# Performance work log

Measured on AMD Instinct MI355X. Metric: run time of the kernel, lower is better.

The kernel has to match this reference:

```python
import jax, jax.numpy as jnp
import numpy as np

NEG_INF = -9e15


def setup_inputs() -> dict:
    key = jax.random.key(0)
    k1, k2, k3, k4, k5 = jax.random.split(key, 5)
    N, F_IN, F_OUT = 8192, 512, 256
    x = jax.random.normal(k1, (N, F_IN), dtype=jnp.float32)
    adjacent_matrix = jax.random.randint(k2, (N, N), 0, 2, dtype=jnp.int32)
    # xavier-normal-like scales (gain sqrt(2))
    W = jax.random.normal(k3, (F_IN, F_OUT), dtype=jnp.float32) * np.sqrt(2.0) * np.sqrt(2.0 / (F_IN + F_OUT))
    a1 = jax.random.normal(k4, (F_OUT, 1), dtype=jnp.float32) * np.sqrt(2.0) * np.sqrt(2.0 / (F_OUT + 1))
    a2 = jax.random.normal(k5, (F_OUT, 1), dtype=jnp.float32) * np.sqrt(2.0) * np.sqrt(2.0 / (F_OUT + 1))
    return {"x": x, "adjacent_matrix": adjacent_matrix, "W": W, "a1": a1, "a2": a2}


def reference(x, adjacent_matrix, W, a1, a2):
    alpha = 0.2  # LeakyReLU negative slope
    h = x @ W                                   # [N, F_out]
    f1 = h @ a1                                 # [N, 1]
    f2 = h @ a2                                 # [N, 1]
    e = f1 + f2.T                               # [N, N] broadcast pairwise scores
    e = jnp.where(e > 0, e, alpha * e)          # LeakyReLU
    e = jnp.where(adjacent_matrix > 0, e, NEG_INF)  # mask non-edges
    attention = jax.nn.softmax(e, axis=1)       # [N, N]
    h_prime = attention @ h                     # [N, F_out]
    return jax.nn.elu(h_prime)                  # concat=True -> ELU
```

## Files before the change

kernel.cpp:

```cpp
#include <hip/hip_runtime.h>
#include <hip/hip_bf16.h>

#define N_NODES 8192
#define F_IN 512
#define F_OUT 256
#define KSPLIT 4
#define KCHUNK (N_NODES / KSPLIT)

using short8 = __attribute__((ext_vector_type(8))) short;
using f32x4  = __attribute__((ext_vector_type(4))) float;

__device__ __forceinline__ short f2bf(float v) {
    union { float f; unsigned u; } x; x.f = v;
    unsigned r = x.u + 0x7fffu + ((x.u >> 16) & 1u);
    return (short)(r >> 16);
}

__global__ void k_prep(const float* __restrict__ W, const float* __restrict__ a1,
                       const float* __restrict__ a2, float* __restrict__ w1,
                       float* __restrict__ w2, short* __restrict__ WTg) {
    const int k = blockIdx.x;
    const int l = threadIdx.x;
    float4 wv = *(const float4*)(W + (size_t)k * F_OUT + 4 * l);
    float4 av = *(const float4*)(a1 + 4 * l);
    float4 bv = *(const float4*)(a2 + 4 * l);
    float s1 = wv.x*av.x + wv.y*av.y + wv.z*av.z + wv.w*av.w;
    float s2 = wv.x*bv.x + wv.y*bv.y + wv.z*bv.z + wv.w*bv.w;
    WTg[(size_t)(4*l+0)*F_IN + k] = f2bf(wv.x);
    WTg[(size_t)(4*l+1)*F_IN + k] = f2bf(wv.y);
    WTg[(size_t)(4*l+2)*F_IN + k] = f2bf(wv.z);
    WTg[(size_t)(4*l+3)*F_IN + k] = f2bf(wv.w);
    #pragma unroll
    for (int off = 32; off; off >>= 1) {
        s1 += __shfl_down(s1, off);
        s2 += __shfl_down(s2, off);
    }
    if (l == 0) { w1[k] = s1; w2[k] = s2; }
}

__global__ void k_f12(const float* __restrict__ x, const float* __restrict__ w1,
                      const float* __restrict__ w2, float* __restrict__ f1,
                      float* __restrict__ f2) {
    const int wv = threadIdx.x >> 6, l = threadIdx.x & 63;
    const int i = blockIdx.x * 4 + wv;
    const float* xr = x + (size_t)i * F_IN;
    float s1 = 0.f, s2 = 0.f;
    #pragma unroll
    for (int t = 0; t < 2; ++t) {
        int k = t * 256 + l * 4;
        float4 xv = *(const float4*)(xr + k);
        float4 u  = *(const float4*)(w1 + k);
        float4 v  = *(const float4*)(w2 + k);
        s1 += xv.x*u.x + xv.y*u.y + xv.z*u.z + xv.w*u.w;
        s2 += xv.x*v.x + xv.y*v.y + xv.z*v.z + xv.w*v.w;
    }
    #pragma unroll
    for (int off = 32; off; off >>= 1) {
        s1 += __shfl_down(s1, off);
        s2 += __shfl_down(s2, off);
    }
    if (l == 0) { f1[i] = s1; f2[i] = s2; }
}

__global__ void k_f2max(const float* __restrict__ f2, float* __restrict__ F2max) {
    const int t = threadIdx.x;
    float m = -3.4e38f;
    for (int i = t; i < N_NODES; i += 1024) m = fmaxf(m, f2[i]);
    #pragma unroll
    for (int off = 32; off; off >>= 1) m = fmaxf(m, __shfl_down(m, off));
    __shared__ float sm[16];
    if ((t & 63) == 0) sm[t >> 6] = m;
    __syncthreads();
    if (t == 0) {
        float mm = sm[0];
        #pragma unroll
        for (int w = 1; w < 16; ++w) mm = fmaxf(mm, sm[w]);
        *F2max = mm;
    }
}

__launch_bounds__(256)
__global__ void k_hT(const float* __restrict__ x, const short* __restrict__ WTg,
                     short* __restrict__ hT) {
    __shared__ short x_lds[32 * 64];
    __shared__ short wt_lds[256 * 64];
    const int tid = threadIdx.x;
    const int wv = tid >> 6, l = tid & 63, lg = l >> 4, lr = l & 15;
    const int ibase = blockIdx.x * 32;
    f32x4 acc[4][2];
    #pragma unroll
    for (int a = 0; a < 4; ++a)
        #pragma unroll
        for (int b = 0; b < 2; ++b) acc[a][b] = (f32x4){0.f, 0.f, 0.f, 0.f};
    for (int k0 = 0; k0 < F_IN; k0 += 64) {
        __syncthreads();
        {
            int i = tid >> 3, ch = tid & 7;
            const float* src = x + (size_t)(ibase + i) * F_IN + k0 + ch * 8;
            float4 v0 = *(const float4*)(src);
            float4 v1 = *(const float4*)(src + 4);
            short8 s;
            s[0]=f2bf(v0.x); s[1]=f2bf(v0.y); s[2]=f2bf(v0.z); s[3]=f2bf(v0.w);
            s[4]=f2bf(v1.x); s[5]=f2bf(v1.y); s[6]=f2bf(v1.z); s[7]=f2bf(v1.w);
            *(short8*)&x_lds[i * 64 + 8 * (ch ^ (i & 7))] = s;
        }
        {
            int cb = tid >> 3, ch = tid & 7;
            #pragma unroll
            for (int p = 0; p < 8; ++p) {
                int c = cb + 32 * p;
                short8 s = *(const short8*)(WTg + (size_t)c * F_IN + k0 + ch * 8);
                *(short8*)&wt_lds[c * 64 + 8 * (ch ^ (c & 7))] = s;
            }
        }
        __syncthreads();
        #pragma unroll
        for (int ks = 0; ks < 2; ++ks) {
            short8 bfrag[2], afrag[4];
            #pragma unroll
            for (int it = 0; it < 2; ++it) {
                int i = it * 16 + lr;
                bfrag[it] = *(short8*)&x_lds[i * 64 + 8 * ((lg + 4*ks) ^ (i & 7))];
            }
            #pragma unroll
            for (int ct = 0; ct < 4; ++ct) {
                int c = wv * 64 + ct * 16 + lr;
                afrag[ct] = *(short8*)&wt_lds[c * 64 + 8 * ((lg + 4*ks) ^ (c & 7))];
            }
            #pragma unroll
            for (int ct = 0; ct < 4; ++ct)
                #pragma unroll
                for (int it = 0; it < 2; ++it)
                    acc[ct][it] = __builtin_amdgcn_mfma_f32_16x16x32_bf16(
                        afrag[ct], bfrag[it], acc[ct][it], 0, 0, 0);
        }
    }
    #pragma unroll
    for (int ct = 0; ct < 4; ++ct)
        #pragma unroll
        for (int it = 0; it < 2; ++it)
            #pragma unroll
            for (int r = 0; r < 4; ++r) {
                int c = wv * 64 + ct * 16 + 4 * lg + r;
                int i = ibase + it * 16 + lr;
                hT[(size_t)c * N_NODES + i] = f2bf(acc[ct][it][r]);
            }
}

__launch_bounds__(256)
__global__ void k_attn(const int* __restrict__ adj, const short* __restrict__ hT,
                       const float* __restrict__ f1, const float* __restrict__ f2,
                       const float* __restrict__ F2maxp, float* __restrict__ part,
                       float* __restrict__ psum) {
    __shared__ short h_lds[256 * 64];
    const int tid = threadIdx.x;
    const int wv = tid >> 6, l = tid & 63, lg = l >> 4, lr = l & 15;
    const int ksid = blockIdx.x >> 7;
    const int rowblk = blockIdx.x & 127;
    const int r0 = rowblk * 64;
    const int myrow = r0 + wv * 16 + lr;
    const float F2m = *F2maxp;
    const float f1v = f1[myrow];
    const float e0 = f1v + F2m;
    const float cr = fmaxf(e0, 0.2f * e0);
    const float L2E = 1.44269504f;
    const float crl = cr * L2E;
    f32x4 acc[16];
    #pragma unroll
    for (int t = 0; t < 16; ++t) acc[t] = (f32x4){0.f, 0.f, 0.f, 0.f};
    float ps = 0.f;
    const int kbeg = ksid * KCHUNK;
    const int* arow = adj + (size_t)myrow * N_NODES;
    for (int k0 = kbeg; k0 < kbeg + KCHUNK; k0 += 64) {
        __syncthreads();
        {
            int cb = tid >> 3, ch = tid & 7;
            #pragma unroll
            for (int p = 0; p < 8; ++p) {
                int c = cb + 32 * p;
                short8 s = *(const short8*)(hT + (size_t)c * N_NODES + k0 + ch * 8);
                *(short8*)&h_lds[c * 64 + 8 * (ch ^ (c & 7))] = s;
            }
        }
        __syncthreads();
        #pragma unroll
        for (int ks = 0; ks < 2; ++ks) {
            const int kg = k0 + 32 * ks + 8 * lg;
            const int4 av0 = *(const int4*)(arow + kg);
            const int4 av1 = *(const int4*)(arow + kg + 4);
            const float4 fa = *(const float4*)(f2 + kg);
            const float4 fb = *(const float4*)(f2 + kg + 4);
            const float f2v[8] = {fa.x, fa.y, fa.z, fa.w, fb.x, fb.y, fb.z, fb.w};
            const int   am[8]  = {av0.x, av0.y, av0.z, av0.w, av1.x, av1.y, av1.z, av1.w};
            short8 pa;
            #pragma unroll
            for (int j = 0; j < 8; ++j) {
                float ee = f1v + f2v[j];
                float le = fmaxf(ee, 0.2f * ee);
                float pv = (am[j] > 0) ? exp2f(fmaf(le, L2E, -crl)) : 0.f;
                ps += pv;
                pa[j] = f2bf(pv);
            }
            #pragma unroll
            for (int t = 0; t < 16; ++t) {
                int c = t * 16 + lr;
                short8 bfrag = *(short8*)&h_lds[c * 64 + 8 * ((lg + 4*ks) ^ (c & 7))];
                acc[t] = __builtin_amdgcn_mfma_f32_16x16x32_bf16(pa, bfrag, acc[t], 0, 0, 0);
            }
        }
    }
    ps += __shfl_xor(ps, 16);
    ps += __shfl_xor(ps, 32);
    if (lg == 0) psum[ksid * N_NODES + myrow] = ps;
    float* pb = part + (size_t)ksid * N_NODES * F_OUT;
    #pragma unroll
    for (int t = 0; t < 16; ++t)
        #pragma unroll
        for (int r = 0; r < 4; ++r) {
            int row = r0 + wv * 16 + 4 * lg + r;
            int c = t * 16 + lr;
            pb[(size_t)row * F_OUT + c] = acc[t][r];
        }
}

__global__ void k_comb(const float* __restrict__ part, const float* __restrict__ psum,
                       float* __restrict__ out) {
    const int i = blockIdx.x, c = threadIdx.x;
    float o = 0.f, s = 0.f;
    #pragma unroll
    for (int q = 0; q < KSPLIT; ++q) {
        o += part[(size_t)q * N_NODES * F_OUT + (size_t)i * F_OUT + c];
        s += psum[q * N_NODES + i];
    }
    float v = o / s;
    out[(size_t)i * F_OUT + c] = (v > 0.f) ? v : expm1f(v);
}

extern "C" void kernel_launch(void* const* d_in, const int* in_sizes, int n_in,
                              void* d_out, int out_size, void* d_ws, size_t ws_size,
                              hipStream_t stream) {
    const float* x  = (const float*)d_in[0];
    const int* adj  = (const int*)d_in[1];
    const float* W  = (const float*)d_in[2];
    const float* a1 = (const float*)d_in[3];
    const float* a2 = (const float*)d_in[4];
    float* out = (float*)d_out;

    short* hT  = (short*)d_ws;
    short* WTg = hT + (size_t)F_OUT * N_NODES;
    float* fb  = (float*)(WTg + (size_t)F_OUT * F_IN);
    float* w1   = fb;
    float* w2   = fb + 512;
    float* f1   = fb + 1024;
    float* f2   = fb + 1024 + N_NODES;
    float* F2m  = fb + 1024 + 2 * N_NODES;
    float* part = fb + 32768;
    float* psum = part + (size_t)KSPLIT * N_NODES * F_OUT;

    k_prep<<<F_IN, 64, 0, stream>>>(W, a1, a2, w1, w2, WTg);
    k_f12<<<N_NODES / 4, 256, 0, stream>>>(x, w1, w2, f1, f2);
    k_f2max<<<1, 1024, 0, stream>>>(f2, F2m);
    k_hT<<<N_NODES / 32, 256, 0, stream>>>(x, WTg, hT);
    k_attn<<<128 * KSPLIT, 256, 0, stream>>>(adj, hT, f1, f2, F2m, part, psum);
    k_comb<<<N_NODES, 256, 0, stream>>>(part, psum, out);
}
```

Before: 454.4 us.

## Double-buffer attention tiles in registers, pack adjacency mask, drop max shift

The attention kernel now prefetches the next hT tile and adjacency chunk into registers while the current tile is computed. The adjacency values are compressed into bitmasks in LDS and loaded coalesced, replacing per-lane strided int loads. The per-row max-shift kernel is removed and exponents are clamped to 80 instead, and occupancy is hinted with launch_bounds(256,2). This adds register pressure and relies on the clamp to keep unshifted exp values from overflowing.

```diff
diff --git a/kernel.cpp b/kernel.cpp
--- a/kernel.cpp
+++ b/kernel.cpp
@@ -62,23 +62,6 @@
     if (l == 0) { f1[i] = s1; f2[i] = s2; }
 }
 
-__global__ void k_f2max(const float* __restrict__ f2, float* __restrict__ F2max) {
-    const int t = threadIdx.x;
-    float m = -3.4e38f;
-    for (int i = t; i < N_NODES; i += 1024) m = fmaxf(m, f2[i]);
-    #pragma unroll
-    for (int off = 32; off; off >>= 1) m = fmaxf(m, __shfl_down(m, off));
-    __shared__ float sm[16];
-    if ((t & 63) == 0) sm[t >> 6] = m;
-    __syncthreads();
-    if (t == 0) {
-        float mm = sm[0];
-        #pragma unroll
-        for (int w = 1; w < 16; ++w) mm = fmaxf(mm, sm[w]);
-        *F2max = mm;
-    }
-}
-
 __launch_bounds__(256)
 __global__ void k_hT(const float* __restrict__ x, const short* __restrict__ WTg,
                      short* __restrict__ hT) {
@@ -147,68 +130,109 @@
             }
 }
 
-__launch_bounds__(256)
+__launch_bounds__(256, 2)
 __global__ void k_attn(const int* __restrict__ adj, const short* __restrict__ hT,
                        const float* __restrict__ f1, const float* __restrict__ f2,
-                       const float* __restrict__ F2maxp, float* __restrict__ part,
-                       float* __restrict__ psum) {
+                       float* __restrict__ part, float* __restrict__ psum) {
     __shared__ short h_lds[256 * 64];
+    __shared__ unsigned short am_lds[64 * 4];
     const int tid = threadIdx.x;
     const int wv = tid >> 6, l = tid & 63, lg = l >> 4, lr = l & 15;
     const int ksid = blockIdx.x >> 7;
     const int rowblk = blockIdx.x & 127;
     const int r0 = rowblk * 64;
     const int myrow = r0 + wv * 16 + lr;
-    const float F2m = *F2maxp;
+    const int cb = tid >> 3, ch = tid & 7;
+    const short* hsrc = hT + (size_t)cb * N_NODES + ch * 8;
+    const int hswz = 8 * (ch ^ (cb & 7));
+    const int q = l & 3, srow = wv * 16 + (l >> 2);
+    const int* asrc = adj + (size_t)(r0 + srow) * N_NODES + q * 16;
+    const int srow4 = srow * 4 + q;
+    const int rowm4 = (wv * 16 + lr) * 4;
     const float f1v = f1[myrow];
-    const float e0 = f1v + F2m;
-    const float cr = fmaxf(e0, 0.2f * e0);
     const float L2E = 1.44269504f;
-    const float crl = cr * L2E;
     f32x4 acc[16];
     #pragma unroll
     for (int t = 0; t < 16; ++t) acc[t] = (f32x4){0.f, 0.f, 0.f, 0.f};
     float ps = 0.f;
     const int kbeg = ksid * KCHUNK;
-    const int* arow = adj + (size_t)myrow * N_NODES;
-    for (int k0 = kbeg; k0 < kbeg + KCHUNK; k0 += 64) {
+    const int kend = kbeg + KCHUNK;
+
+    short8 AH[8], BH[8];
+    int4   AA[4], BA[4];
+
+#define LOADT(K0, H, A) do {                                                   \
+    _Pragma("unroll")                                                          \
+    for (int p = 0; p < 8; ++p)                                                \
+        H[p] = *(const short8*)(hsrc + (size_t)(32 * p) * N_NODES + (K0));     \
+    _Pragma("unroll")                                                          \
+    for (int p = 0; p < 4; ++p)                                                \
+        A[p] = *(const int4*)(asrc + (K0) + p * 4);                            \
+} while (0)
+
+#define WRITET(H, A) do {                                                      \
+    _Pragma("unroll")                                                          \
+    for (int p = 0; p < 8; ++p)                                                \
+        *(short8*)&h_lds[(cb + 32 * p) * 64 + hswz] = H[p];                    \
+    unsigned m = 0;                                                            \
+    _Pragma("unroll")                                                          \
+    for (int p = 0; p < 4; ++p) {                                              \
+        m |= (A[p].x > 0 ? 1u : 0u) << (4 * p);                                \
+        m |= (A[p].y > 0 ? 2u : 0u) << (4 * p);                                \
+        m |= (A[p].z > 0 ? 4u : 0u) << (4 * p);                                \
+        m |= (A[p].w > 0 ? 8u : 0u) << (4 * p);                                \
+    }                                                                          \
+    am_lds[srow4] = (unsigned short)m;                                         \
+} while (0)
+
+#define COMPUTE(K0) do {                                                       \
+    _Pragma("unroll")                                                          \
+    for (int ks = 0; ks < 2; ++ks) {                                           \
+        const int kg = (K0) + 32 * ks + 8 * lg;                                \
+        const unsigned am = am_lds[rowm4 + 2 * ks + (lg >> 1)];                \
+        const unsigned mbyte = (am >> (8 * (lg & 1))) & 0xffu;                 \
+        const float4 fa = *(const float4*)(f2 + kg);                           \
+        const float4 fb = *(const float4*)(f2 + kg + 4);                       \
+        const float f2v[8] = {fa.x, fa.y, fa.z, fa.w, fb.x, fb.y, fb.z, fb.w}; \
+        short8 pa;                                                             \
+        _Pragma("unroll")                                                      \
+        for (int j = 0; j < 8; ++j) {                                          \
+            float ee = f1v + f2v[j];                                           \
+            float le = fmaxf(ee, 0.2f * ee);                                   \
+            float pv = (mbyte & (1u << j))                                     \
+                           ? exp2f(fminf(le * L2E, 80.f)) : 0.f;               \
+            ps += pv;                                                          \
+            pa[j] = f2bf(pv);                                                  \
+        }                                                                      \
+        _Pragma("unroll")                                                      \
+        for (int t = 0; t < 16; ++t) {                                         \
+            const int c = t * 16 + lr;                                         \
+            short8 bfrag = *(short8*)&h_lds[c * 64 + 8 * ((lg + 4*ks) ^ (lr & 7))]; \
+            acc[t] = __builtin_amdgcn_mfma_f32_16x16x32_bf16(pa, bfrag, acc[t], 0, 0, 0); \
+        }                                                                      \
+    }                                                                          \
+} while (0)
+
+    LOADT(kbeg, AH, AA);
+    for (int k0 = kbeg; k0 < kend; k0 += 128) {
+        __syncthreads();
+        WRITET(AH, AA);
+        __syncthreads();
+        LOADT(k0 + 64, BH, BA);
+        COMPUTE(k0);
+        __syncthreads();
+        WRITET(BH, BA);
         __syncthreads();
         {
-            int cb = tid >> 3, ch = tid & 7;
-            #pragma unroll
-            for (int p = 0; p < 8; ++p) {
-                int c = cb + 32 * p;
-                short8 s = *(const short8*)(hT + (size_t)c * N_NODES + k0 + ch * 8);
-                *(short8*)&h_lds[c * 64 + 8 * (ch ^ (c & 7))] = s;
-            }
-        }
-        __syncthreads();
-        #pragma unroll
-        for (int ks = 0; ks < 2; ++ks) {
-            const int kg = k0 + 32 * ks + 8 * lg;
-            const int4 av0 = *(const int4*)(arow + kg);
-            const int4 av1 = *(const int4*)(arow + kg + 4);
-            const float4 fa = *(const float4*)(f2 + kg);
-            const float4 fb = *(const float4*)(f2 + kg + 4);
-            const float f2v[8] = {fa.x, fa.y, fa.z, fa.w, fb.x, fb.y, fb.z, fb.w};
-            const int   am[8]  = {av0.x, av0.y, av0.z, av0.w, av1.x, av1.y, av1.z, av1.w};
-            short8 pa;
-            #pragma unroll
-            for (int j = 0; j < 8; ++j) {
-                float ee = f1v + f2v[j];
-                float le = fmaxf(ee, 0.2f * ee);
-                float pv = (am[j] > 0) ? exp2f(fmaf(le, L2E, -crl)) : 0.f;
-                ps += pv;
-                pa[j] = f2bf(pv);
-            }
-            #pragma unroll
-            for (int t = 0; t < 16; ++t) {
-                int c = t * 16 + lr;
-                short8 bfrag = *(short8*)&h_lds[c * 64 + 8 * ((lg + 4*ks) ^ (c & 7))];
-                acc[t] = __builtin_amdgcn_mfma_f32_16x16x32_bf16(pa, bfrag, acc[t], 0, 0, 0);
-            }
-        }
-    }
+            const int kn = (k0 + 128 < kend) ? (k0 + 128) : kbeg;
+            LOADT(kn, AH, AA);
+        }
+        COMPUTE(k0 + 64);
+    }
+#undef LOADT
+#undef WRITET
+#undef COMPUTE
+
     ps += __shfl_xor(ps, 16);
     ps += __shfl_xor(ps, 32);
     if (lg == 0) psum[ksid * N_NODES + myrow] = ps;
@@ -228,9 +252,9 @@
     const int i = blockIdx.x, c = threadIdx.x;
     float o = 0.f, s = 0.f;
     #pragma unroll
-    for (int q = 0; q < KSPLIT; ++q) {
-        o += part[(size_t)q * N_NODES * F_OUT + (size_t)i * F_OUT + c];
-        s += psum[q * N_NODES + i];
+    for (int qq = 0; qq < KSPLIT; ++qq) {
+        o += part[(size_t)qq * N_NODES * F_OUT + (size_t)i * F_OUT + c];
+        s += psum[qq * N_NODES + i];
     }
     float v = o / s;
     out[(size_t)i * F_OUT + c] = (v > 0.f) ? v : expm1f(v);
@@ -253,14 +277,12 @@
     float* w2   = fb + 512;
     float* f1   = fb + 1024;
     float* f2   = fb + 1024 + N_NODES;
-    float* F2m  = fb + 1024 + 2 * N_NODES;
     float* part = fb + 32768;
     float* psum = part + (size_t)KSPLIT * N_NODES * F_OUT;
 
     k_prep<<<F_IN, 64, 0, stream>>>(W, a1, a2, w1, w2, WTg);
     k_f12<<<N_NODES / 4, 256, 0, stream>>>(x, w1, w2, f1, f2);
-    k_f2max<<<1, 1024, 0, stream>>>(f2, F2m);
     k_hT<<<N_NODES / 32, 256, 0, stream>>>(x, WTg, hT);
-    k_attn<<<128 * KSPLIT, 256, 0, stream>>>(adj, hT, f1, f2, F2m, part, psum);
+    k_attn<<<128 * KSPLIT, 256, 0, stream>>>(adj, hT, f1, f2, part, psum);
     k_comb<<<N_NODES, 256, 0, stream>>>(part, psum, out);
 }
```

Result: slower. 477.8 us (+5.1%).
